# Optimization experiments

Hardware: AMD Instinct MI355X
Metric: run time of the kernel (lower is better)

Reference implementation:

```python
import jax, jax.numpy as jnp
import numpy as np

M, N, C, RED = 12, 8, 1024, 16  # n_routers, num_adapters, model_dim, reduction_factor
D = C // RED                    # down_sample_size = 64
B, S = 32, 512


def setup_inputs() -> dict:
    key = jax.random.key(0)
    k1, k2, k3, k4, k5 = jax.random.split(key, 5)
    x = jax.random.normal(k1, (B, S, C), dtype=jnp.float32)
    expert_index = jax.random.randint(k2, (M, B), 0, N)
    down_w = jax.random.normal(k3, (M, N, C, D), dtype=jnp.float32) * 0.01
    down_b = jnp.zeros((M, N, D), dtype=jnp.float32)
    up_w = jax.random.normal(k4, (M, N, D, C), dtype=jnp.float32) * 0.01
    return {"x": x, "expert_index": expert_index, "down_w": down_w,
            "down_b": down_b, "up_w": up_w}


def reference(x, expert_index, down_w, down_b, up_w):
    # Hard-routing path: gather per-(router, batch) expert weights, then batched GEMMs.
    m_idx = jnp.arange(M)[:, None]                      # [M,1]
    bw_down = down_w[m_idx, expert_index]               # [M,B,C,D]
    bb_down = down_b[m_idx, expert_index]               # [M,B,D]
    bw_up = up_w[m_idx, expert_index]                   # [M,B,D,C]
    z = jnp.einsum('bsc,mbcd->mbsd', x, bw_down) + bb_down[:, :, None, :]
    z = z * jax.nn.sigmoid(z)                           # swish
    u = jnp.einsum('mbsd,mbdc->mbsc', z, bw_up)         # [M,B,S,C]
    return u
```

## Files before the change

### kernel.cpp

```cpp
#include <hip/hip_runtime.h>

#define M_R   12
#define N_E   8
#define C_DIM 1024
#define D_DIM 64
#define B_SZ  32
#define S_SZ  512
#define TS    128
#define PAD   72

typedef __bf16 bf16x8 __attribute__((ext_vector_type(8)));
typedef float  floatx4 __attribute__((ext_vector_type(4)));

__device__ __forceinline__ unsigned short f2bf(float f) {
    unsigned int u = __float_as_uint(f);
    u += 0x7FFFu + ((u >> 16) & 1u);
    return (unsigned short)(u >> 16);
}

__global__ __launch_bounds__(256) void adapter_fused(
    const float* __restrict__ x,
    const int*   __restrict__ eidx,
    const float* __restrict__ down_w,
    const float* __restrict__ down_b,
    const float* __restrict__ up_w,
    float*       __restrict__ out)
{
    __shared__ unsigned short Xs[TS * PAD];
    __shared__ unsigned short Wt[D_DIM * PAD];
    __shared__ float bias_s[D_DIM];

    const int t    = threadIdx.x;
    const int wave = t >> 6;
    const int lane = t & 63;
    const int l15  = lane & 15;
    const int quad = lane >> 4;
    const int srow = wave * 32;

    const int bid = blockIdx.x;
    const int m  = bid % M_R;
    const int p  = bid / M_R;
    const int b  = p >> 2;
    const int sc = p & 3;
    const int s0 = sc * TS;

    const int e = eidx[m * B_SZ + b];

    const float* xb   = x      + (b * S_SZ + s0) * C_DIM;
    const float* wd   = down_w + (m * N_E + e) * (C_DIM * D_DIM);
    const float* bias = down_b + (m * N_E + e) * D_DIM;
    const float* wu   = up_w   + (m * N_E + e) * (D_DIM * C_DIM);
    float*       outp = out    + ((m * B_SZ + b) * S_SZ + s0) * C_DIM;

    if (t < D_DIM) bias_s[t] = bias[t];

    floatx4 acc[2][4];
    #pragma unroll
    for (int i = 0; i < 2; ++i)
        #pragma unroll
        for (int j = 0; j < 4; ++j)
            acc[i][j] = (floatx4){0.f, 0.f, 0.f, 0.f};

    for (int kk = 0; kk < C_DIM; kk += 64) {
        #pragma unroll
        for (int i = 0; i < 8; ++i) {
            int f4 = i * 256 + t;
            int s  = f4 >> 4;
            int k4 = (f4 & 15) << 2;
            float4 v = *(const float4*)(xb + s * C_DIM + kk + k4);
            ushort4 h;
            h.x = f2bf(v.x); h.y = f2bf(v.y); h.z = f2bf(v.z); h.w = f2bf(v.w);
            *(ushort4*)&Xs[s * PAD + k4] = h;
        }
        #pragma unroll
        for (int i = 0; i < 4; ++i) {
            int f4 = i * 256 + t;
            int c  = f4 >> 4;
            int d4 = (f4 & 15) << 2;
            float4 v = *(const float4*)(wd + (kk + c) * D_DIM + d4);
            Wt[(d4 + 0) * PAD + c] = f2bf(v.x);
            Wt[(d4 + 1) * PAD + c] = f2bf(v.y);
            Wt[(d4 + 2) * PAD + c] = f2bf(v.z);
            Wt[(d4 + 3) * PAD + c] = f2bf(v.w);
        }
        __syncthreads();

        #pragma unroll
        for (int ks = 0; ks < 64; ks += 32) {
            bf16x8 a0 = *(const bf16x8*)&Xs[(srow +      l15) * PAD + ks + quad * 8];
            bf16x8 a1 = *(const bf16x8*)&Xs[(srow + 16 + l15) * PAD + ks + quad * 8];
            #pragma unroll
            for (int nt = 0; nt < 4; ++nt) {
                bf16x8 bf = *(const bf16x8*)&Wt[(nt * 16 + l15) * PAD + ks + quad * 8];
                acc[0][nt] = __builtin_amdgcn_mfma_f32_16x16x32_bf16(a0, bf, acc[0][nt], 0, 0, 0);
                acc[1][nt] = __builtin_amdgcn_mfma_f32_16x16x32_bf16(a1, bf, acc[1][nt], 0, 0, 0);
            }
        }
        __syncthreads();
    }

    #pragma unroll
    for (int mt = 0; mt < 2; ++mt)
        #pragma unroll
        for (int nt = 0; nt < 4; ++nt)
            #pragma unroll
            for (int r = 0; r < 4; ++r) {
                float z  = acc[mt][nt][r] + bias_s[nt * 16 + l15];
                float sw = z / (1.0f + __expf(-z));
                int s = srow + mt * 16 + quad * 4 + r;
                int d = nt * 16 + l15;
                Xs[s * PAD + d] = f2bf(sw);
            }
    __syncthreads();

    bf16x8 za[2][2];
    #pragma unroll
    for (int mt = 0; mt < 2; ++mt)
        #pragma unroll
        for (int ki = 0; ki < 2; ++ki)
            za[mt][ki] = *(const bf16x8*)&Xs[(srow + mt * 16 + l15) * PAD + ki * 32 + quad * 8];

    for (int ci = 0; ci < 16; ++ci) {
        int c0 = ci * 64;
        #pragma unroll
        for (int i = 0; i < 4; ++i) {
            int f4 = i * 256 + t;
            int d  = f4 >> 4;
            int c4 = (f4 & 15) << 2;
            float4 v = *(const float4*)(wu + d * C_DIM + c0 + c4);
            Wt[(c4 + 0) * PAD + d] = f2bf(v.x);
            Wt[(c4 + 1) * PAD + d] = f2bf(v.y);
            Wt[(c4 + 2) * PAD + d] = f2bf(v.z);
            Wt[(c4 + 3) * PAD + d] = f2bf(v.w);
        }
        __syncthreads();

        floatx4 acc2[2][4];
        #pragma unroll
        for (int i = 0; i < 2; ++i)
            #pragma unroll
            for (int j = 0; j < 4; ++j)
                acc2[i][j] = (floatx4){0.f, 0.f, 0.f, 0.f};

        #pragma unroll
        for (int ki = 0; ki < 2; ++ki) {
            #pragma unroll
            for (int nt = 0; nt < 4; ++nt) {
                bf16x8 bf = *(const bf16x8*)&Wt[(nt * 16 + l15) * PAD + ki * 32 + quad * 8];
                acc2[0][nt] = __builtin_amdgcn_mfma_f32_16x16x32_bf16(za[0][ki], bf, acc2[0][nt], 0, 0, 0);
                acc2[1][nt] = __builtin_amdgcn_mfma_f32_16x16x32_bf16(za[1][ki], bf, acc2[1][nt], 0, 0, 0);
            }
        }

        #pragma unroll
        for (int mt = 0; mt < 2; ++mt)
            #pragma unroll
            for (int nt = 0; nt < 4; ++nt)
                #pragma unroll
                for (int r = 0; r < 4; ++r) {
                    int s = srow + mt * 16 + quad * 4 + r;
                    int c = c0 + nt * 16 + l15;
                    outp[s * C_DIM + c] = acc2[mt][nt][r];
                }
        __syncthreads();
    }
}

extern "C" void kernel_launch(void* const* d_in, const int* in_sizes, int n_in,
                              void* d_out, int out_size, void* d_ws, size_t ws_size,
                              hipStream_t stream) {
    const float* x      = (const float*)d_in[0];
    const int*   eidx   = (const int*)d_in[1];
    const float* down_w = (const float*)d_in[2];
    const float* down_b = (const float*)d_in[3];
    const float* up_w   = (const float*)d_in[4];
    float*       out    = (float*)d_out;

    const int grid = M_R * B_SZ * (S_SZ / TS);
    adapter_fused<<<grid, 256, 0, stream>>>(x, eidx, down_w, down_b, up_w, out);
}
```

Baseline: 1.078 ms.

## Pre-convert inputs and weights to bf16 in workspace and read fragments from global memory

Adds three pre-pass kernels that convert x to bf16 and transpose/convert down and up weights to bf16 into the workspace. The main kernel then loads MFMA fragments straight from global or L2 memory instead of staging through LDS each k-step. This removes the repeated fp32 loads and conversions that every block was redoing (x is reread by 12 routers), and drops most barriers. The cost is extra launches, about 130MB of extra traffic, and uncoalesced fragment loads. It falls back to the old kernel if the workspace is too small.

```diff
diff --git a/kernel.cpp b/kernel.cpp
--- a/kernel.cpp
+++ b/kernel.cpp
@@ -16,6 +16,193 @@
     unsigned int u = __float_as_uint(f);
     u += 0x7FFFu + ((u >> 16) & 1u);
     return (unsigned short)(u >> 16);
+}
+
+__global__ __launch_bounds__(256) void cvt_x(const float* __restrict__ x,
+                                             unsigned short* __restrict__ xb) {
+    const int i = blockIdx.x * 256 + threadIdx.x;
+    const float4* p = (const float4*)x + (size_t)i * 2;
+    float4 a = p[0], b = p[1];
+    unsigned short h[8] __attribute__((aligned(16)));
+    h[0] = f2bf(a.x); h[1] = f2bf(a.y); h[2] = f2bf(a.z); h[3] = f2bf(a.w);
+    h[4] = f2bf(b.x); h[5] = f2bf(b.y); h[6] = f2bf(b.z); h[7] = f2bf(b.w);
+    ((uint4*)xb)[i] = *(const uint4*)h;
+}
+
+__global__ __launch_bounds__(256) void cvt_wd(const float* __restrict__ wd,
+                                              unsigned short* __restrict__ wdT) {
+    __shared__ unsigned short T[64 * 65];
+    const int blk   = blockIdx.x;
+    const int slice = blk >> 4;
+    const int c0    = (blk & 15) * 64;
+    const float*    src = wd  + (size_t)slice * (C_DIM * D_DIM);
+    unsigned short* dst = wdT + (size_t)slice * (C_DIM * D_DIM);
+    const int t = threadIdx.x;
+
+    #pragma unroll
+    for (int i = 0; i < 4; ++i) {
+        int f4 = i * 256 + t;
+        int c  = f4 >> 4;
+        int d4 = (f4 & 15) << 2;
+        float4 v = *(const float4*)(src + (size_t)(c0 + c) * D_DIM + d4);
+        T[(d4 + 0) * 65 + c] = f2bf(v.x);
+        T[(d4 + 1) * 65 + c] = f2bf(v.y);
+        T[(d4 + 2) * 65 + c] = f2bf(v.z);
+        T[(d4 + 3) * 65 + c] = f2bf(v.w);
+    }
+    __syncthreads();
+    const int d   = t >> 2;
+    const int c16 = (t & 3) << 4;
+    unsigned short tmp[16] __attribute__((aligned(16)));
+    #pragma unroll
+    for (int j = 0; j < 16; ++j) tmp[j] = T[d * 65 + c16 + j];
+    *(uint4*)(dst + (size_t)d * C_DIM + c0 + c16)     = ((const uint4*)tmp)[0];
+    *(uint4*)(dst + (size_t)d * C_DIM + c0 + c16 + 8) = ((const uint4*)tmp)[1];
+}
+
+__global__ __launch_bounds__(256) void cvt_wu(const float* __restrict__ wu,
+                                              unsigned short* __restrict__ wuT) {
+    __shared__ unsigned short T[64 * 65];
+    const int blk   = blockIdx.x;
+    const int slice = blk >> 4;
+    const int c0    = (blk & 15) * 64;
+    const float*    src = wu  + (size_t)slice * (D_DIM * C_DIM);
+    unsigned short* dst = wuT + (size_t)slice * (D_DIM * C_DIM);
+    const int t = threadIdx.x;
+
+    #pragma unroll
+    for (int i = 0; i < 4; ++i) {
+        int f4 = i * 256 + t;
+        int d  = f4 >> 4;
+        int c4 = (f4 & 15) << 2;
+        float4 v = *(const float4*)(src + (size_t)d * C_DIM + c0 + c4);
+        T[(c4 + 0) * 65 + d] = f2bf(v.x);
+        T[(c4 + 1) * 65 + d] = f2bf(v.y);
+        T[(c4 + 2) * 65 + d] = f2bf(v.z);
+        T[(c4 + 3) * 65 + d] = f2bf(v.w);
+    }
+    __syncthreads();
+    const int c   = t >> 2;
+    const int d16 = (t & 3) << 4;
+    unsigned short tmp[16] __attribute__((aligned(16)));
+    #pragma unroll
+    for (int j = 0; j < 16; ++j) tmp[j] = T[c * 65 + d16 + j];
+    *(uint4*)(dst + (size_t)(c0 + c) * D_DIM + d16)     = ((const uint4*)tmp)[0];
+    *(uint4*)(dst + (size_t)(c0 + c) * D_DIM + d16 + 8) = ((const uint4*)tmp)[1];
+}
+
+__global__ __launch_bounds__(256) void adapter_fused_v2(
+    const unsigned short* __restrict__ xb_all,
+    const int*            __restrict__ eidx,
+    const unsigned short* __restrict__ wdT,
+    const float*          __restrict__ down_b,
+    const unsigned short* __restrict__ wuT,
+    float*                __restrict__ out)
+{
+    __shared__ unsigned short Zs[TS * PAD];
+
+    const int t    = threadIdx.x;
+    const int wave = t >> 6;
+    const int lane = t & 63;
+    const int l15  = lane & 15;
+    const int quad = lane >> 4;
+    const int srow = wave * 32;
+
+    const int bid = blockIdx.x;
+    const int m  = bid % M_R;
+    const int p  = bid / M_R;
+    const int b  = p >> 2;
+    const int sc = p & 3;
+    const int s0 = sc * TS;
+
+    const int e = eidx[m * B_SZ + b];
+
+    const unsigned short* xb   = xb_all + ((size_t)(b * S_SZ + s0)) * C_DIM;
+    const unsigned short* wd   = wdT    + (size_t)(m * N_E + e) * (C_DIM * D_DIM);
+    const float*          bias = down_b + (size_t)(m * N_E + e) * D_DIM;
+    const unsigned short* wu   = wuT    + (size_t)(m * N_E + e) * (C_DIM * D_DIM);
+    float*                outp = out    + ((size_t)((m * B_SZ + b) * S_SZ + s0)) * C_DIM;
+
+    floatx4 acc[2][4];
+    #pragma unroll
+    for (int i = 0; i < 2; ++i)
+        #pragma unroll
+        for (int j = 0; j < 4; ++j)
+            acc[i][j] = (floatx4){0.f, 0.f, 0.f, 0.f};
+
+    #pragma unroll 2
+    for (int kk = 0; kk < C_DIM; kk += 64) {
+        #pragma unroll
+        for (int ks = 0; ks < 64; ks += 32) {
+            const int k = kk + ks + quad * 8;
+            bf16x8 a0 = *(const bf16x8*)(xb + (size_t)(srow +      l15) * C_DIM + k);
+            bf16x8 a1 = *(const bf16x8*)(xb + (size_t)(srow + 16 + l15) * C_DIM + k);
+            #pragma unroll
+            for (int nt = 0; nt < 4; ++nt) {
+                bf16x8 bf = *(const bf16x8*)(wd + (size_t)(nt * 16 + l15) * C_DIM + k);
+                acc[0][nt] = __builtin_amdgcn_mfma_f32_16x16x32_bf16(a0, bf, acc[0][nt], 0, 0, 0);
+                acc[1][nt] = __builtin_amdgcn_mfma_f32_16x16x32_bf16(a1, bf, acc[1][nt], 0, 0, 0);
+            }
+        }
+    }
+
+    float bv[4];
+    #pragma unroll
+    for (int nt = 0; nt < 4; ++nt) bv[nt] = bias[nt * 16 + l15];
+
+    #pragma unroll
+    for (int mt = 0; mt < 2; ++mt)
+        #pragma unroll
+        for (int nt = 0; nt < 4; ++nt)
+            #pragma unroll
+            for (int r = 0; r < 4; ++r) {
+                float z  = acc[mt][nt][r] + bv[nt];
+                float sw = z / (1.0f + __expf(-z));
+                int s = srow + mt * 16 + quad * 4 + r;
+                int d = nt * 16 + l15;
+                Zs[s * PAD + d] = f2bf(sw);
+            }
+    __syncthreads();
+
+    bf16x8 za[2][2];
+    #pragma unroll
+    for (int mt = 0; mt < 2; ++mt)
+        #pragma unroll
+        for (int ki = 0; ki < 2; ++ki)
+            za[mt][ki] = *(const bf16x8*)&Zs[(srow + mt * 16 + l15) * PAD + ki * 32 + quad * 8];
+
+    for (int ci = 0; ci < 16; ++ci) {
+        const int c0 = ci * 64;
+
+        floatx4 acc2[2][4];
+        #pragma unroll
+        for (int i = 0; i < 2; ++i)
+            #pragma unroll
+            for (int j = 0; j < 4; ++j)
+                acc2[i][j] = (floatx4){0.f, 0.f, 0.f, 0.f};
+
+        #pragma unroll
+        for (int ki = 0; ki < 2; ++ki) {
+            #pragma unroll
+            for (int nt = 0; nt < 4; ++nt) {
+                bf16x8 bf = *(const bf16x8*)(wu + (size_t)(c0 + nt * 16 + l15) * D_DIM
+                                                + ki * 32 + quad * 8);
+                acc2[0][nt] = __builtin_amdgcn_mfma_f32_16x16x32_bf16(za[0][ki], bf, acc2[0][nt], 0, 0, 0);
+                acc2[1][nt] = __builtin_amdgcn_mfma_f32_16x16x32_bf16(za[1][ki], bf, acc2[1][nt], 0, 0, 0);
+            }
+        }
+
+        #pragma unroll
+        for (int mt = 0; mt < 2; ++mt)
+            #pragma unroll
+            for (int nt = 0; nt < 4; ++nt)
+                #pragma unroll
+                for (int r = 0; r < 4; ++r) {
+                    int s = srow + mt * 16 + quad * 4 + r;
+                    int c = c0 + nt * 16 + l15;
+                    outp[(size_t)s * C_DIM + c] = acc2[mt][nt][r];
+                }
+    }
 }
 
 __global__ __launch_bounds__(256) void adapter_fused(
@@ -177,5 +364,21 @@
     float*       out    = (float*)d_out;
 
     const int grid = M_R * B_SZ * (S_SZ / TS);
-    adapter_fused<<<grid, 256, 0, stream>>>(x, eidx, down_w, down_b, up_w, out);
-}
+
+    const size_t XBE = (size_t)B_SZ * S_SZ * C_DIM;
+    const size_t WE  = (size_t)M_R * N_E * C_DIM * D_DIM;
+    const size_t REQ = (XBE + 2 * WE) * sizeof(unsigned short);
+
+    if (d_ws != nullptr && ws_size >= REQ) {
+        unsigned short* xb  = (unsigned short*)d_ws;
+        unsigned short* wdt = xb  + XBE;
+        unsigned short* wut = wdt + WE;
+
+        cvt_x <<<(int)(XBE / 8 / 256), 256, 0, stream>>>(x, xb);
+        cvt_wd<<<M_R * N_E * 16,       256, 0, stream>>>(down_w, wdt);
+        cvt_wu<<<M_R * N_E * 16,       256, 0, stream>>>(up_w,   wut);
+        adapter_fused_v2<<<grid, 256, 0, stream>>>(xb, eidx, wdt, down_b, wut, out);
+    } else {
+        adapter_fused<<<grid, 256, 0, stream>>>(x, eidx, down_w, down_b, up_w, out);
+    }
+}
```

Measured after the change: 1.067 ms. No clear change (-1.0%).
